# Kernel tuning notes

Hardware: AMD Instinct MI355X
Metric: run time of the kernel (lower is better)

## Reference

```python
import jax, jax.numpy as jnp
import numpy as np

B, N, D, K = 16, 512, 256, 12  # batch, nodes, node_dim, num edge types (4 arg + 4 arg' + punct +/- + no_edges +/-)
ITERATION_STEPS = 1


def setup_inputs() -> dict:
    key = jax.random.key(0)
    ks = jax.random.split(key, 8)
    node = jax.random.normal(ks[0], (B, N, D), dtype=jnp.float32)
    node_mask = jax.random.randint(ks[1], (B, N), 0, 2, dtype=jnp.int32)
    graphs = jax.random.randint(ks[2], (K, B, N, N), 0, 2, dtype=jnp.int32)
    s = 1.0 / np.sqrt(D)
    Ww = jax.random.normal(ks[3], (1, D), dtype=jnp.float32) * s   # _node_weight_fc
    bw = jnp.zeros((1,), dtype=jnp.float32)
    Ws = jax.random.normal(ks[4], (D, D), dtype=jnp.float32) * s   # _self_node_fc
    bs = jnp.zeros((D,), dtype=jnp.float32)
    Wk = jax.random.normal(ks[5], (K, D, D), dtype=jnp.float32) * s  # 12 bias-free per-edge-type linears
    return {"node": node, "Ww": Ww, "bw": bw, "Ws": Ws, "bs": bs, "Wk": Wk,
            "node_mask": node_mask, "graphs": graphs}


def reference(node, Ww, bw, Ws, bs, Wk, node_mask, graphs):
    dt = node.dtype
    mask = node_mask.astype(dt)
    eye = jnp.eye(N, dtype=dt)
    # dd_graph = mask_row * mask_col * (1 - diag)
    dd = mask[:, None, :] * mask[:, :, None] * (1.0 - eye)          # [B,N,N]
    g = dd[None] * graphs.astype(dt)                                # [K,B,N,N] masked adjacencies
    neigh = g.sum(axis=(0, 3))                                      # [B,N] total neighbor count
    neigh = jnp.where(neigh >= 1, neigh, jnp.ones((), dt))

    all_w = []
    for _ in range(ITERATION_STEPS):
        # (1) node relatedness
        w = jax.nn.sigmoid(node @ Ww.T + bw)[..., 0]                # [B,N]
        all_w.append(w)
        self_info = node @ Ws.T + bs                                # [B,N,D]
        # (2) message propagation for all 12 edge types, batched
        trans = jnp.einsum('bnd,ked->kbne', node, Wk)               # [K,B,N,D] per-type linear (x @ W.T)
        wg = w[None, :, None, :] * g                                # [K,B,N,N] masked node weights
        agg = jnp.einsum('kbmn,kbnd->bmd', wg, trans) / neigh[..., None]
        # (3) update
        node = jax.nn.relu(self_info + agg)

    all_weight = jnp.stack(all_w, axis=1)                           # [B,steps,N]
    return node, all_weight
```

## Files before the change

kernel.cpp:

```cpp
#include <hip/hip_runtime.h>
#include <hip/hip_bf16.h>
#include <math.h>

#define BB 16
#define NN 512
#define DD 256
#define KK 12

typedef __bf16 bf16x8 __attribute__((ext_vector_type(8)));
typedef __bf16 bf16x4 __attribute__((ext_vector_type(4)));
typedef float  f32x4  __attribute__((ext_vector_type(4)));

#define WS_WM     0
#define WS_NCNT   32768
#define WS_NODEBF 65536
#define WS_NODET  4259840
#define WS_WKBF   8454144
#define WS_WSBF   10027008
#define WS_T      10158080

__global__ __launch_bounds__(256) void k1_prep(const float* __restrict__ node,
        const float* __restrict__ Ww, const float* __restrict__ bw,
        const int* __restrict__ node_mask,
        float* __restrict__ wm, __bf16* __restrict__ node_bf,
        float* __restrict__ all_w) {
    int t = threadIdx.x;
    int lane = t & 63;
    int row = blockIdx.x * 4 + (t >> 6);
    const float4 nv = *(const float4*)(node + (size_t)row * DD + lane * 4);
    const float4 wv = *(const float4*)(Ww + lane * 4);
    float dot = nv.x*wv.x + nv.y*wv.y + nv.z*wv.z + nv.w*wv.w;
    #pragma unroll
    for (int off = 32; off > 0; off >>= 1) dot += __shfl_xor(dot, off);
    float w = 1.0f / (1.0f + expf(-(dot + bw[0])));
    int mk = node_mask[row];
    if (lane == 0) {
        wm[row]    = w * (float)mk;
        all_w[row] = w;
    }
    bf16x4 nb = {(__bf16)nv.x, (__bf16)nv.y, (__bf16)nv.z, (__bf16)nv.w};
    *(bf16x4*)(node_bf + (size_t)row * DD + lane * 4) = nb;
}

__global__ __launch_bounds__(256) void k1b_convert(const float* __restrict__ Wk,
        const float* __restrict__ Ws, __bf16* __restrict__ Wk_bf, __bf16* __restrict__ Ws_bf) {
    const int KDD = KK * DD * DD;
    int idx = (blockIdx.x * 256 + threadIdx.x) * 4;
    if (idx < KDD) {
        float4 v = *(const float4*)(Wk + idx);
        bf16x4 o = {(__bf16)v.x, (__bf16)v.y, (__bf16)v.z, (__bf16)v.w};
        *(bf16x4*)(Wk_bf + idx) = o;
    } else {
        int j = idx - KDD;
        if (j < DD * DD) {
            float4 v = *(const float4*)(Ws + j);
            bf16x4 o = {(__bf16)v.x, (__bf16)v.y, (__bf16)v.z, (__bf16)v.w};
            *(bf16x4*)(Ws_bf + j) = o;
        }
    }
}

__global__ __launch_bounds__(256) void k2_transpose(const __bf16* __restrict__ src,
                                                    __bf16* __restrict__ dst) {
    __shared__ __bf16 tile[64][65];
    int bx = blockIdx.x;
    int b = bx >> 5; int rest = bx & 31; int nt = rest >> 2; int dt = rest & 3;
    int n0 = nt * 64, d0 = dt * 64;
    int t = threadIdx.x;
    #pragma unroll
    for (int i = 0; i < 16; i++) {
        int idx = i * 256 + t;
        int n = idx >> 6, d = idx & 63;
        tile[n][d] = src[((size_t)(b * NN + n0 + n)) * DD + d0 + d];
    }
    __syncthreads();
    #pragma unroll
    for (int i = 0; i < 16; i++) {
        int idx = i * 256 + t;
        int d = idx >> 6, n = idx & 63;
        dst[((size_t)(b * DD + d0 + d)) * NN + n0 + n] = tile[n][d];
    }
}

__global__ __launch_bounds__(256) void k4_stageA(const int* __restrict__ graphs,
        const float* __restrict__ wm, const __bf16* __restrict__ node_t,
        __bf16* __restrict__ T, int* __restrict__ ncnt) {
    __shared__ __align__(16) __bf16 Asub[64][72];
    __shared__ __align__(16) __bf16 Bsub[256][72];
    int bx = blockIdx.x;
    int mt = bx & 7;
    int kb = bx >> 3;
    int b = kb & 15;
    int k = kb >> 4;
    int m0 = mt * 64;
    int t = threadIdx.x;
    int lane = t & 63;
    int wave = t >> 6;
    int q = lane >> 4;
    int l16 = lane & 15;

    f32x4 acc[4][4];
    #pragma unroll
    for (int i = 0; i < 4; i++)
        #pragma unroll
        for (int j = 0; j < 4; j++) acc[i][j] = (f32x4){0.f, 0.f, 0.f, 0.f};

    int am = t >> 2;
    int aq = t & 3;
    const int* grow = graphs + ((size_t)((k * BB + b) * NN + m0 + am)) * NN;
    int mg = m0 + am;
    int bd = t >> 2;
    int bq = t & 3;
    int cnt = 0;

    for (int n0 = 0; n0 < NN; n0 += 64) {
        #pragma unroll
        for (int i = 0; i < 4; i++) {
            int nbase = n0 + aq * 16 + i * 4;
            int4 g = *(const int4*)(grow + nbase);
            float4 w4 = *(const float4*)(wm + b * NN + nbase);
            bool v0ok = (nbase + 0 != mg) && (w4.x != 0.0f);
            bool v1ok = (nbase + 1 != mg) && (w4.y != 0.0f);
            bool v2ok = (nbase + 2 != mg) && (w4.z != 0.0f);
            bool v3ok = (nbase + 3 != mg) && (w4.w != 0.0f);
            cnt += (v0ok ? g.x : 0) + (v1ok ? g.y : 0) + (v2ok ? g.z : 0) + (v3ok ? g.w : 0);
            __bf16 v0 = (__bf16)(v0ok ? (float)g.x * w4.x : 0.0f);
            __bf16 v1 = (__bf16)(v1ok ? (float)g.y * w4.y : 0.0f);
            __bf16 v2 = (__bf16)(v2ok ? (float)g.z * w4.z : 0.0f);
            __bf16 v3 = (__bf16)(v3ok ? (float)g.w * w4.w : 0.0f);
            bf16x4 pack = {v0, v1, v2, v3};
            *(bf16x4*)&Asub[am][aq * 16 + i * 4] = pack;
        }
        #pragma unroll
        for (int p = 0; p < 4; p++) {
            int d = bd + p * 64;
            const __bf16* src = node_t + ((size_t)(b * DD + d)) * NN + n0 + bq * 16;
            bf16x8 u0 = *(const bf16x8*)(src);
            bf16x8 u1 = *(const bf16x8*)(src + 8);
            *(bf16x8*)&Bsub[d][bq * 16]     = u0;
            *(bf16x8*)&Bsub[d][bq * 16 + 8] = u1;
        }
        __syncthreads();
        bf16x8 af[4][2], bfr[4][2];
        #pragma unroll
        for (int fm = 0; fm < 4; fm++)
            #pragma unroll
            for (int kk = 0; kk < 2; kk++)
                af[fm][kk] = *(const bf16x8*)&Asub[fm * 16 + l16][kk * 32 + q * 8];
        #pragma unroll
        for (int fd = 0; fd < 4; fd++)
            #pragma unroll
            for (int kk = 0; kk < 2; kk++)
                bfr[fd][kk] = *(const bf16x8*)&Bsub[wave * 64 + fd * 16 + l16][kk * 32 + q * 8];
        #pragma unroll
        for (int fm = 0; fm < 4; fm++)
            #pragma unroll
            for (int fd = 0; fd < 4; fd++)
                #pragma unroll
                for (int kk = 0; kk < 2; kk++)
                    acc[fm][fd] = __builtin_amdgcn_mfma_f32_16x16x32_bf16(
                        af[fm][kk], bfr[fd][kk], acc[fm][fd], 0, 0, 0);
        __syncthreads();
    }
    cnt += __shfl_xor(cnt, 1);
    cnt += __shfl_xor(cnt, 2);
    if ((t & 3) == 0) atomicAdd(&ncnt[b * NN + mg], cnt);

    #pragma unroll
    for (int fm = 0; fm < 4; fm++)
        #pragma unroll
        for (int fd = 0; fd < 4; fd++) {
            int col = wave * 64 + fd * 16 + l16;
            #pragma unroll
            for (int r = 0; r < 4; r++) {
                int m = m0 + fm * 16 + q * 4 + r;
                T[((size_t)((b * NN + m) * KK + k)) * DD + col] = (__bf16)acc[fm][fd][r];
            }
        }
}

__global__ __launch_bounds__(256) void k5_stageB(const __bf16* __restrict__ T,
        const __bf16* __restrict__ Wk_bf, const __bf16* __restrict__ node_bf,
        const __bf16* __restrict__ Ws_bf, const float* __restrict__ bs,
        const int* __restrict__ ncnt, const int* __restrict__ node_mask,
        float* __restrict__ out) {
    __shared__ __align__(16) __bf16 Asub[64][136];
    __shared__ __align__(16) __bf16 Bsub[128][136];
    int bx = blockIdx.x;
    int rt = bx & 127;
    int dt = bx >> 7;
    int b  = rt >> 3;
    int m0 = (rt & 7) * 64;
    int t = threadIdx.x;
    int lane = t & 63;
    int wave = t >> 6;
    int wm2 = wave >> 1;
    int wd2 = wave & 1;
    int q = lane >> 4;
    int l16 = lane & 15;

    f32x4 acc[2][4];
    #pragma unroll
    for (int i = 0; i < 2; i++)
        #pragma unroll
        for (int j = 0; j < 4; j++) acc[i][j] = (f32x4){0.f, 0.f, 0.f, 0.f};

    int ar = t >> 2; int ac = (t & 3) * 32;
    int br = t >> 1; int bc = (t & 1) * 64;

    const __bf16* Arow = T + (size_t)(b * NN + m0 + ar) * (KK * DD);
    const __bf16* Brow0 = Wk_bf + (size_t)(dt * 128 + br) * DD;

    for (int it = 0; it < 24; it++) {
        int kred0 = it * 128;
        int k = it >> 1;
        int e0 = (it & 1) * 128;
        const __bf16* asrc = Arow + kred0 + ac;
        #pragma unroll
        for (int i = 0; i < 4; i++)
            *(bf16x8*)&Asub[ar][ac + i * 8] = *(const bf16x8*)(asrc + i * 8);
        const __bf16* bsrc = Brow0 + (size_t)k * DD * DD + e0 + bc;
        #pragma unroll
        for (int i = 0; i < 8; i++)
            *(bf16x8*)&Bsub[br][bc + i * 8] = *(const bf16x8*)(bsrc + i * 8);
        __syncthreads();
        #pragma unroll
        for (int kk = 0; kk < 4; kk++) {
            bf16x8 af[2], bfr[4];
            #pragma unroll
            for (int fm = 0; fm < 2; fm++)
                af[fm] = *(const bf16x8*)&Asub[wm2 * 32 + fm * 16 + l16][kk * 32 + q * 8];
            #pragma unroll
            for (int fd = 0; fd < 4; fd++)
                bfr[fd] = *(const bf16x8*)&Bsub[wd2 * 64 + fd * 16 + l16][kk * 32 + q * 8];
            #pragma unroll
            for (int fm = 0; fm < 2; fm++)
                #pragma unroll
                for (int fd = 0; fd < 4; fd++)
                    acc[fm][fd] = __builtin_amdgcn_mfma_f32_16x16x32_bf16(
                        af[fm], bfr[fd], acc[fm][fd], 0, 0, 0);
        }
        __syncthreads();
    }

    #pragma unroll
    for (int fm = 0; fm < 2; fm++) {
        #pragma unroll
        for (int r = 0; r < 4; r++) {
            int m = m0 + wm2 * 32 + fm * 16 + q * 4 + r;
            int mk = node_mask[b * NN + m];
            int c  = ncnt[b * NN + m];
            float s = (float)mk / (float)(c >= 1 ? c : 1);
            #pragma unroll
            for (int fd = 0; fd < 4; fd++) acc[fm][fd][r] *= s;
        }
    }

    const __bf16* ArowS = node_bf + (size_t)(b * NN + m0 + ar) * DD;
    const __bf16* BrowS = Ws_bf + (size_t)(dt * 128 + br) * DD;
    for (int si = 0; si < 2; si++) {
        int e0 = si * 128;
        const __bf16* asrc = ArowS + e0 + ac;
        #pragma unroll
        for (int i = 0; i < 4; i++)
            *(bf16x8*)&Asub[ar][ac + i * 8] = *(const bf16x8*)(asrc + i * 8);
        const __bf16* bsrc = BrowS + e0 + bc;
        #pragma unroll
        for (int i = 0; i < 8; i++)
            *(bf16x8*)&Bsub[br][bc + i * 8] = *(const bf16x8*)(bsrc + i * 8);
        __syncthreads();
        #pragma unroll
        for (int kk = 0; kk < 4; kk++) {
            bf16x8 af[2], bfr[4];
            #pragma unroll
            for (int fm = 0; fm < 2; fm++)
                af[fm] = *(const bf16x8*)&Asub[wm2 * 32 + fm * 16 + l16][kk * 32 + q * 8];
            #pragma unroll
            for (int fd = 0; fd < 4; fd++)
                bfr[fd] = *(const bf16x8*)&Bsub[wd2 * 64 + fd * 16 + l16][kk * 32 + q * 8];
            #pragma unroll
            for (int fm = 0; fm < 2; fm++)
                #pragma unroll
                for (int fd = 0; fd < 4; fd++)
                    acc[fm][fd] = __builtin_amdgcn_mfma_f32_16x16x32_bf16(
                        af[fm], bfr[fd], acc[fm][fd], 0, 0, 0);
        }
        __syncthreads();
    }

    #pragma unroll
    for (int fm = 0; fm < 2; fm++)
        #pragma unroll
        for (int fd = 0; fd < 4; fd++) {
            int d = dt * 128 + wd2 * 64 + fd * 16 + l16;
            float bsv = bs[d];
            #pragma unroll
            for (int r = 0; r < 4; r++) {
                int m = m0 + wm2 * 32 + fm * 16 + q * 4 + r;
                float v = acc[fm][fd][r] + bsv;
                out[((size_t)(b * NN + m)) * DD + d] = fmaxf(v, 0.0f);
            }
        }
}

extern "C" void kernel_launch(void* const* d_in, const int* in_sizes, int n_in,
                              void* d_out, int out_size, void* d_ws, size_t ws_size,
                              hipStream_t stream) {
    const float* node      = (const float*)d_in[0];
    const float* Ww        = (const float*)d_in[1];
    const float* bw        = (const float*)d_in[2];
    const float* Ws        = (const float*)d_in[3];
    const float* bs        = (const float*)d_in[4];
    const float* Wk        = (const float*)d_in[5];
    const int*   node_mask = (const int*)d_in[6];
    const int*   graphs    = (const int*)d_in[7];
    float* out   = (float*)d_out;
    float* all_w = out + (size_t)BB * NN * DD;

    char* ws = (char*)d_ws;
    float*  wm      = (float*)(ws + WS_WM);
    int*    ncnt    = (int*)(ws + WS_NCNT);
    __bf16* node_bf = (__bf16*)(ws + WS_NODEBF);
    __bf16* node_t  = (__bf16*)(ws + WS_NODET);
    __bf16* Wk_bf   = (__bf16*)(ws + WS_WKBF);
    __bf16* Ws_bf   = (__bf16*)(ws + WS_WSBF);
    __bf16* Tbuf    = (__bf16*)(ws + WS_T);

    hipMemsetAsync(ncnt, 0, BB * NN * sizeof(int), stream);
    k1_prep    <<<2048, 256, 0, stream>>>(node, Ww, bw, node_mask, wm, node_bf, all_w);
    k1b_convert<<< 832, 256, 0, stream>>>(Wk, Ws, Wk_bf, Ws_bf);
    k2_transpose<<<512, 256, 0, stream>>>(node_bf, node_t);
    k4_stageA  <<<1536, 256, 0, stream>>>(graphs, wm, node_t, Tbuf, ncnt);
    k5_stageB  <<< 256, 256, 0, stream>>>(Tbuf, Wk_bf, node_bf, Ws_bf, bs, ncnt, node_mask, out);
}
```

Measured before the change: 380.9 us.

## Fold node weights into transposed features and load MFMA operands directly from global

The node weight w (which already carries the mask) is now multiplied into the transposed bf16 node features instead of into the adjacency tile. Stage A therefore builds its A tile from the raw 0/1 graph with packed integer tricks that give bf16 1.0 directly, and counts neighbors using the mask. Stage A's B operand and all of stage B's operands are read straight from global memory, with no LDS staging. Stage B splits the reduction dimension across waves and sums the partials in a shared buffer, running twice as many blocks. This cuts LDS traffic and per-element float work, at the cost of uncoalesced global operand loads and a serialized cross-wave reduction.

```diff
diff --git a/kernel.cpp b/kernel.cpp
--- a/kernel.cpp
+++ b/kernel.cpp
@@ -60,9 +60,9 @@
     }
 }
 
-__global__ __launch_bounds__(256) void k2_transpose(const __bf16* __restrict__ src,
-                                                    __bf16* __restrict__ dst) {
-    __shared__ __bf16 tile[64][65];
+__global__ __launch_bounds__(256) void k2_transpose(const float* __restrict__ node,
+        const float* __restrict__ wm, __bf16* __restrict__ dst) {
+    __shared__ float tile[64][65];
     int bx = blockIdx.x;
     int b = bx >> 5; int rest = bx & 31; int nt = rest >> 2; int dt = rest & 3;
     int n0 = nt * 64, d0 = dt * 64;
@@ -71,22 +71,22 @@
     for (int i = 0; i < 16; i++) {
         int idx = i * 256 + t;
         int n = idx >> 6, d = idx & 63;
-        tile[n][d] = src[((size_t)(b * NN + n0 + n)) * DD + d0 + d];
+        tile[n][d] = node[((size_t)(b * NN + n0 + n)) * DD + d0 + d];
     }
     __syncthreads();
     #pragma unroll
     for (int i = 0; i < 16; i++) {
         int idx = i * 256 + t;
         int d = idx >> 6, n = idx & 63;
-        dst[((size_t)(b * DD + d0 + d)) * NN + n0 + n] = tile[n][d];
+        float w = wm[b * NN + n0 + n];
+        dst[((size_t)(b * DD + d0 + d)) * NN + n0 + n] = (__bf16)(tile[n][d] * w);
     }
 }
 
 __global__ __launch_bounds__(256) void k4_stageA(const int* __restrict__ graphs,
-        const float* __restrict__ wm, const __bf16* __restrict__ node_t,
+        const int* __restrict__ node_mask, const __bf16* __restrict__ node_t,
         __bf16* __restrict__ T, int* __restrict__ ncnt) {
     __shared__ __align__(16) __bf16 Asub[64][72];
-    __shared__ __align__(16) __bf16 Bsub[256][72];
     int bx = blockIdx.x;
     int mt = bx & 7;
     int kb = bx >> 3;
@@ -98,6 +98,7 @@
     int wave = t >> 6;
     int q = lane >> 4;
     int l16 = lane & 15;
+    int e0 = wave * 64;
 
     f32x4 acc[4][4];
     #pragma unroll
@@ -108,69 +109,63 @@
     int am = t >> 2;
     int aq = t & 3;
     const int* grow = graphs + ((size_t)((k * BB + b) * NN + m0 + am)) * NN;
+    const int* mrow = node_mask + b * NN;
     int mg = m0 + am;
-    int bd = t >> 2;
-    int bq = t & 3;
-    int cnt = 0;
+    unsigned cnt = 0;
 
     for (int n0 = 0; n0 < NN; n0 += 64) {
         #pragma unroll
         for (int i = 0; i < 4; i++) {
             int nbase = n0 + aq * 16 + i * 4;
-            int4 g = *(const int4*)(grow + nbase);
-            float4 w4 = *(const float4*)(wm + b * NN + nbase);
-            bool v0ok = (nbase + 0 != mg) && (w4.x != 0.0f);
-            bool v1ok = (nbase + 1 != mg) && (w4.y != 0.0f);
-            bool v2ok = (nbase + 2 != mg) && (w4.z != 0.0f);
-            bool v3ok = (nbase + 3 != mg) && (w4.w != 0.0f);
-            cnt += (v0ok ? g.x : 0) + (v1ok ? g.y : 0) + (v2ok ? g.z : 0) + (v3ok ? g.w : 0);
-            __bf16 v0 = (__bf16)(v0ok ? (float)g.x * w4.x : 0.0f);
-            __bf16 v1 = (__bf16)(v1ok ? (float)g.y * w4.y : 0.0f);
-            __bf16 v2 = (__bf16)(v2ok ? (float)g.z * w4.z : 0.0f);
-            __bf16 v3 = (__bf16)(v3ok ? (float)g.w * w4.w : 0.0f);
-            bf16x4 pack = {v0, v1, v2, v3};
-            *(bf16x4*)&Asub[am][aq * 16 + i * 4] = pack;
-        }
-        #pragma unroll
-        for (int p = 0; p < 4; p++) {
-            int d = bd + p * 64;
-            const __bf16* src = node_t + ((size_t)(b * DD + d)) * NN + n0 + bq * 16;
-            bf16x8 u0 = *(const bf16x8*)(src);
-            bf16x8 u1 = *(const bf16x8*)(src + 8);
-            *(bf16x8*)&Bsub[d][bq * 16]     = u0;
-            *(bf16x8*)&Bsub[d][bq * 16 + 8] = u1;
+            int4 g  = *(const int4*)(grow + nbase);
+            int4 mk = *(const int4*)(mrow + nbase);
+            unsigned p0 = (unsigned)g.x | ((unsigned)g.y << 16);
+            unsigned p1 = (unsigned)g.z | ((unsigned)g.w << 16);
+            unsigned drel = (unsigned)(mg - nbase);
+            if (drel < 4u) {
+                unsigned bit = 1u << (16 * (drel & 1));
+                if (drel < 2u) p0 &= ~bit; else p1 &= ~bit;
+            }
+            unsigned mp0 = (unsigned)mk.x | ((unsigned)mk.y << 16);
+            unsigned mp1 = (unsigned)mk.z | ((unsigned)mk.w << 16);
+            cnt += (p0 & mp0) + (p1 & mp1);
+            uint2 st;
+            st.x = p0 * 0x3F80u;
+            st.y = p1 * 0x3F80u;
+            *(uint2*)&Asub[am][aq * 16 + i * 4] = st;
         }
         __syncthreads();
-        bf16x8 af[4][2], bfr[4][2];
-        #pragma unroll
-        for (int fm = 0; fm < 4; fm++)
-            #pragma unroll
-            for (int kk = 0; kk < 2; kk++)
-                af[fm][kk] = *(const bf16x8*)&Asub[fm * 16 + l16][kk * 32 + q * 8];
-        #pragma unroll
-        for (int fd = 0; fd < 4; fd++)
-            #pragma unroll
-            for (int kk = 0; kk < 2; kk++)
-                bfr[fd][kk] = *(const bf16x8*)&Bsub[wave * 64 + fd * 16 + l16][kk * 32 + q * 8];
-        #pragma unroll
-        for (int fm = 0; fm < 4; fm++)
+        #pragma unroll
+        for (int kk = 0; kk < 2; kk++) {
+            bf16x8 af[4], bfr[4];
+            #pragma unroll
+            for (int fm = 0; fm < 4; fm++)
+                af[fm] = *(const bf16x8*)&Asub[fm * 16 + l16][kk * 32 + q * 8];
             #pragma unroll
             for (int fd = 0; fd < 4; fd++)
+                bfr[fd] = *(const bf16x8*)(node_t +
+                    ((size_t)(b * DD + e0 + fd * 16 + l16)) * NN + n0 + kk * 32 + q * 8);
+            #pragma unroll
+            for (int fm = 0; fm < 4; fm++)
                 #pragma unroll
-                for (int kk = 0; kk < 2; kk++)
+                for (int fd = 0; fd < 4; fd++)
                     acc[fm][fd] = __builtin_amdgcn_mfma_f32_16x16x32_bf16(
-                        af[fm][kk], bfr[fd][kk], acc[fm][fd], 0, 0, 0);
+                        af[fm], bfr[fd], acc[fm][fd], 0, 0, 0);
+        }
         __syncthreads();
     }
-    cnt += __shfl_xor(cnt, 1);
-    cnt += __shfl_xor(cnt, 2);
-    if ((t & 3) == 0) atomicAdd(&ncnt[b * NN + mg], cnt);
+
+    cnt = (cnt & 0xFFFFu) + (cnt >> 16);
+    int ci = (int)cnt;
+    ci += __shfl_xor(ci, 1);
+    ci += __shfl_xor(ci, 2);
+    if (aq == 0) atomicAdd(&ncnt[b * NN + mg], ci);
 
     #pragma unroll
     for (int fm = 0; fm < 4; fm++)
         #pragma unroll
         for (int fd = 0; fd < 4; fd++) {
-            int col = wave * 64 + fd * 16 + l16;
+            int col = e0 + fd * 16 + l16;
             #pragma unroll
             for (int r = 0; r < 4; r++) {
                 int m = m0 + fm * 16 + q * 4 + r;
@@ -184,123 +179,108 @@
         const __bf16* __restrict__ Ws_bf, const float* __restrict__ bs,
         const int* __restrict__ ncnt, const int* __restrict__ node_mask,
         float* __restrict__ out) {
-    __shared__ __align__(16) __bf16 Asub[64][136];
-    __shared__ __align__(16) __bf16 Bsub[128][136];
+    __shared__ float redbuf[64][65];
     int bx = blockIdx.x;
-    int rt = bx & 127;
-    int dt = bx >> 7;
-    int b  = rt >> 3;
-    int m0 = (rt & 7) * 64;
+    int b = bx >> 5; int rest = bx & 31; int mt = rest >> 2; int dt = rest & 3;
+    int m0 = mt * 64, d0 = dt * 64;
     int t = threadIdx.x;
     int lane = t & 63;
     int wave = t >> 6;
-    int wm2 = wave >> 1;
-    int wd2 = wave & 1;
     int q = lane >> 4;
     int l16 = lane & 15;
-
-    f32x4 acc[2][4];
-    #pragma unroll
-    for (int i = 0; i < 2; i++)
+    int ew = wave * 64;
+
+    f32x4 acc[4][4];
+    #pragma unroll
+    for (int i = 0; i < 4; i++)
         #pragma unroll
         for (int j = 0; j < 4; j++) acc[i][j] = (f32x4){0.f, 0.f, 0.f, 0.f};
 
-    int ar = t >> 2; int ac = (t & 3) * 32;
-    int br = t >> 1; int bc = (t & 1) * 64;
-
-    const __bf16* Arow = T + (size_t)(b * NN + m0 + ar) * (KK * DD);
-    const __bf16* Brow0 = Wk_bf + (size_t)(dt * 128 + br) * DD;
-
-    for (int it = 0; it < 24; it++) {
-        int kred0 = it * 128;
-        int k = it >> 1;
-        int e0 = (it & 1) * 128;
-        const __bf16* asrc = Arow + kred0 + ac;
-        #pragma unroll
-        for (int i = 0; i < 4; i++)
-            *(bf16x8*)&Asub[ar][ac + i * 8] = *(const bf16x8*)(asrc + i * 8);
-        const __bf16* bsrc = Brow0 + (size_t)k * DD * DD + e0 + bc;
-        #pragma unroll
-        for (int i = 0; i < 8; i++)
-            *(bf16x8*)&Bsub[br][bc + i * 8] = *(const bf16x8*)(bsrc + i * 8);
-        __syncthreads();
-        #pragma unroll
-        for (int kk = 0; kk < 4; kk++) {
-            bf16x8 af[2], bfr[4];
-            #pragma unroll
-            for (int fm = 0; fm < 2; fm++)
-                af[fm] = *(const bf16x8*)&Asub[wm2 * 32 + fm * 16 + l16][kk * 32 + q * 8];
+    for (int k = 0; k < KK; k++) {
+        #pragma unroll
+        for (int kk = 0; kk < 2; kk++) {
+            int eoff = ew + kk * 32 + q * 8;
+            bf16x8 af[4], bfr[4];
+            #pragma unroll
+            for (int fm = 0; fm < 4; fm++)
+                af[fm] = *(const bf16x8*)(T +
+                    ((size_t)(b * NN + m0 + fm * 16 + l16)) * (KK * DD) + k * DD + eoff);
             #pragma unroll
             for (int fd = 0; fd < 4; fd++)
-                bfr[fd] = *(const bf16x8*)&Bsub[wd2 * 64 + fd * 16 + l16][kk * 32 + q * 8];
-            #pragma unroll
-            for (int fm = 0; fm < 2; fm++)
+                bfr[fd] = *(const bf16x8*)(Wk_bf +
+                    ((size_t)(k * DD + d0 + fd * 16 + l16)) * DD + eoff);
+            #pragma unroll
+            for (int fm = 0; fm < 4; fm++)
                 #pragma unroll
                 for (int fd = 0; fd < 4; fd++)
                     acc[fm][fd] = __builtin_amdgcn_mfma_f32_16x16x32_bf16(
                         af[fm], bfr[fd], acc[fm][fd], 0, 0, 0);
         }
+    }
+
+    #pragma unroll
+    for (int fm = 0; fm < 4; fm++) {
+        #pragma unroll
+        for (int r = 0; r < 4; r++) {
+            int m = m0 + fm * 16 + q * 4 + r;
+            int c = ncnt[b * NN + m];
+            float s = (float)node_mask[b * NN + m] / (float)(c >= 1 ? c : 1);
+            #pragma unroll
+            for (int fd = 0; fd < 4; fd++) acc[fm][fd][r] *= s;
+        }
+    }
+
+    #pragma unroll
+    for (int kk = 0; kk < 2; kk++) {
+        int eoff = ew + kk * 32 + q * 8;
+        bf16x8 af[4], bfr[4];
+        #pragma unroll
+        for (int fm = 0; fm < 4; fm++)
+            af[fm] = *(const bf16x8*)(node_bf +
+                ((size_t)(b * NN + m0 + fm * 16 + l16)) * DD + eoff);
+        #pragma unroll
+        for (int fd = 0; fd < 4; fd++)
+            bfr[fd] = *(const bf16x8*)(Ws_bf +
+                ((size_t)(d0 + fd * 16 + l16)) * DD + eoff);
+        #pragma unroll
+        for (int fm = 0; fm < 4; fm++)
+            #pragma unroll
+            for (int fd = 0; fd < 4; fd++)
+                acc[fm][fd] = __builtin_amdgcn_mfma_f32_16x16x32_bf16(
+                    af[fm], bfr[fd], acc[fm][fd], 0, 0, 0);
+    }
+
+    for (int w = 0; w < 4; w++) {
+        if (wave == w) {
+            #pragma unroll
+            for (int fm = 0; fm < 4; fm++)
+                #pragma unroll
+                for (int fd = 0; fd < 4; fd++) {
+                    int dd2 = fd * 16 + l16;
+                    #pragma unroll
+                    for (int r = 0; r < 4; r++) {
+                        int mm = fm * 16 + q * 4 + r;
+                        if (w == 0) redbuf[mm][dd2] = acc[fm][fd][r];
+                        else        redbuf[mm][dd2] += acc[fm][fd][r];
+                    }
+                }
+        }
         __syncthreads();
     }
 
-    #pragma unroll
-    for (int fm = 0; fm < 2; fm++) {
-        #pragma unroll
-        for (int r = 0; r < 4; r++) {
-            int m = m0 + wm2 * 32 + fm * 16 + q * 4 + r;
-            int mk = node_mask[b * NN + m];
-            int c  = ncnt[b * NN + m];
-            float s = (float)mk / (float)(c >= 1 ? c : 1);
-            #pragma unroll
-            for (int fd = 0; fd < 4; fd++) acc[fm][fd][r] *= s;
-        }
-    }
-
-    const __bf16* ArowS = node_bf + (size_t)(b * NN + m0 + ar) * DD;
-    const __bf16* BrowS = Ws_bf + (size_t)(dt * 128 + br) * DD;
-    for (int si = 0; si < 2; si++) {
-        int e0 = si * 128;
-        const __bf16* asrc = ArowS + e0 + ac;
-        #pragma unroll
-        for (int i = 0; i < 4; i++)
-            *(bf16x8*)&Asub[ar][ac + i * 8] = *(const bf16x8*)(asrc + i * 8);
-        const __bf16* bsrc = BrowS + e0 + bc;
-        #pragma unroll
-        for (int i = 0; i < 8; i++)
-            *(bf16x8*)&Bsub[br][bc + i * 8] = *(const bf16x8*)(bsrc + i * 8);
-        __syncthreads();
-        #pragma unroll
-        for (int kk = 0; kk < 4; kk++) {
-            bf16x8 af[2], bfr[4];
-            #pragma unroll
-            for (int fm = 0; fm < 2; fm++)
-                af[fm] = *(const bf16x8*)&Asub[wm2 * 32 + fm * 16 + l16][kk * 32 + q * 8];
-            #pragma unroll
-            for (int fd = 0; fd < 4; fd++)
-                bfr[fd] = *(const bf16x8*)&Bsub[wd2 * 64 + fd * 16 + l16][kk * 32 + q * 8];
-            #pragma unroll
-            for (int fm = 0; fm < 2; fm++)
-                #pragma unroll
-                for (int fd = 0; fd < 4; fd++)
-                    acc[fm][fd] = __builtin_amdgcn_mfma_f32_16x16x32_bf16(
-                        af[fm], bfr[fd], acc[fm][fd], 0, 0, 0);
-        }
-        __syncthreads();
-    }
-
-    #pragma unroll
-    for (int fm = 0; fm < 2; fm++)
-        #pragma unroll
-        for (int fd = 0; fd < 4; fd++) {
-            int d = dt * 128 + wd2 * 64 + fd * 16 + l16;
-            float bsv = bs[d];
-            #pragma unroll
-            for (int r = 0; r < 4; r++) {
-                int m = m0 + wm2 * 32 + fm * 16 + q * 4 + r;
-                float v = acc[fm][fd][r] + bsv;
-                out[((size_t)(b * NN + m)) * DD + d] = fmaxf(v, 0.0f);
-            }
-        }
+    int row = t >> 2;
+    int c0 = (t & 3) * 16;
+    #pragma unroll
+    for (int j = 0; j < 4; j++) {
+        int d = d0 + c0 + j * 4;
+        float4 bv = *(const float4*)(bs + d);
+        float4 v;
+        v.x = fmaxf(redbuf[row][c0 + j * 4 + 0] + bv.x, 0.0f);
+        v.y = fmaxf(redbuf[row][c0 + j * 4 + 1] + bv.y, 0.0f);
+        v.z = fmaxf(redbuf[row][c0 + j * 4 + 2] + bv.z, 0.0f);
+        v.w = fmaxf(redbuf[row][c0 + j * 4 + 3] + bv.w, 0.0f);
+        *(float4*)(out + ((size_t)(b * NN + m0 + row)) * DD + d) = v;
+    }
 }
 
 extern "C" void kernel_launch(void* const* d_in, const int* in_sizes, int n_in,
@@ -329,7 +309,7 @@
     hipMemsetAsync(ncnt, 0, BB * NN * sizeof(int), stream);
     k1_prep    <<<2048, 256, 0, stream>>>(node, Ww, bw, node_mask, wm, node_bf, all_w);
     k1b_convert<<< 832, 256, 0, stream>>>(Wk, Ws, Wk_bf, Ws_bf);
-    k2_transpose<<<512, 256, 0, stream>>>(node_bf, node_t);
-    k4_stageA  <<<1536, 256, 0, stream>>>(graphs, wm, node_t, Tbuf, ncnt);
-    k5_stageB  <<< 256, 256, 0, stream>>>(Tbuf, Wk_bf, node_bf, Ws_bf, bs, ncnt, node_mask, out);
-}
+    k2_transpose<<<512, 256, 0, stream>>>(node, wm, node_t);
+    k4_stageA  <<<1536, 256, 0, stream>>>(graphs, node_mask, node_t, Tbuf, ncnt);
+    k5_stageB  <<< 512, 256, 0, stream>>>(Tbuf, Wk_bf, node_bf, Ws_bf, bs, ncnt, node_mask, out);
+}
```

Result: slower. 393.2 us (+3.2%).
